# Optimization experiments

Measured on AMD Instinct MI355X. Metric: run time of the kernel, lower is better.

## Reference

```python
import jax, jax.numpy as jnp
import numpy as np


def setup_inputs() -> dict:
    key = jax.random.key(0)
    k1, k2, k3 = jax.random.split(key, 3)
    B, R, C = 8, 4096, 1024
    input_dim = 1024
    weight_params = jax.random.normal(k1, (B, R, C), dtype=jnp.float32)
    logits = jax.random.normal(k2, (B, input_dim), dtype=jnp.float32)
    score_w = jax.random.normal(k3, (input_dim, 1), dtype=jnp.float32) * (1.0 / np.sqrt(input_dim))
    score_b = jnp.zeros((1,), dtype=jnp.float32)
    return {"weight_params": weight_params, "logits": logits, "score_w": score_w, "score_b": score_b}


def reference(weight_params, logits, score_w, score_b):
    # score_generator: Linear(input_dim -> 1), then sigmoid -> keep fraction
    keep_fraction = jax.nn.sigmoid(logits @ score_w + score_b)  # [B, 1]
    total_row_count = weight_params.shape[-2]
    rows_to_keep = jnp.clip(
        (keep_fraction * total_row_count).astype(jnp.int32), 1, None
    ).squeeze(-1)  # [B]
    # per-row L2 magnitudes
    row_magnitudes = jnp.linalg.norm(weight_params, axis=-1)  # [B, R]
    # descending sort, pick the k-th largest magnitude as threshold
    sorted_magnitudes = jnp.sort(row_magnitudes, axis=-1)[..., ::-1]  # [B, R]
    thresholds = jnp.take_along_axis(
        sorted_magnitudes, (rows_to_keep - 1)[:, None], axis=-1
    )  # [B, 1]
    top_k_row_mask = (row_magnitudes >= thresholds).astype(weight_params.dtype)  # [B, R]
    return weight_params * top_k_row_mask[..., None]
```

## Files before the change

### kernel.cpp

```cpp
#include <hip/hip_runtime.h>
#include <hip/hip_bf16.h>
#include <math.h>

#define B 8
#define R 4096
#define C 1024
#define NROWS (B * R)
#define F4_PER_ROW (C / 4)

typedef float vfloat4 __attribute__((ext_vector_type(4)));

__global__ void k_mags(const float* __restrict__ wp,
                       float* __restrict__ mags) {
    int row  = blockIdx.x * 4 + (threadIdx.x >> 6);
    int lane = threadIdx.x & 63;
    const vfloat4* p = (const vfloat4*)(wp + (size_t)row * C);
    double acc = 0.0;
#pragma unroll
    for (int j = 0; j < 4; ++j) {
        vfloat4 v = p[j * 64 + lane];
        acc += (double)v.x * v.x + (double)v.y * v.y +
               (double)v.z * v.z + (double)v.w * v.w;
    }
    for (int off = 32; off > 0; off >>= 1)
        acc += __shfl_down(acc, off, 64);
    if (lane == 0) mags[row] = (float)sqrt(acc);
}

__global__ void k_select(const float* __restrict__ logits,
                         const float* __restrict__ sw,
                         const float* __restrict__ sb,
                         const float* __restrict__ mags,
                         float* __restrict__ thr) {
    __shared__ unsigned hist[256];
    __shared__ double dred[16];
    __shared__ unsigned sh_prefix;
    __shared__ int sh_krem;

    const int b = blockIdx.x, t = threadIdx.x;
    const int wave = t >> 6, lane = t & 63;

    double a = (double)logits[b * C + t] * (double)sw[t];
    for (int off = 32; off > 0; off >>= 1)
        a += __shfl_down(a, off, 64);
    if (lane == 0) dred[wave] = a;
    __syncthreads();
    if (t == 0) {
        double s = (double)sb[0];
        for (int w = 0; w < 16; ++w) s += dred[w];
        double kf = 1.0 / (1.0 + exp(-s));
        int k = (int)(kf * (double)R);
        if (k < 1) k = 1;
        if (k > R) k = R;
        sh_krem = k;
        sh_prefix = 0u;
    }

    unsigned u[4];
#pragma unroll
    for (int j = 0; j < 4; ++j)
        u[j] = __float_as_uint(mags[b * R + t + j * 1024]);
    __syncthreads();

    const int shifts[4] = {24, 16, 8, 0};
    const unsigned maskH[4] = {0x00000000u, 0xFF000000u, 0xFFFF0000u, 0xFFFFFF00u};
#pragma unroll
    for (int p = 0; p < 4; ++p) {
        const int shift = shifts[p];
        const unsigned mh = maskH[p];
        if (t < 256) hist[t] = 0u;
        __syncthreads();
        const unsigned pref = sh_prefix;
        const int krem = sh_krem;
#pragma unroll
        for (int j = 0; j < 4; ++j) {
            if ((u[j] & mh) == pref)
                atomicAdd(&hist[(u[j] >> shift) & 255u], 1u);
        }
        __syncthreads();
        if (t < 64) {
            unsigned h0 = hist[4 * t], h1 = hist[4 * t + 1],
                     h2 = hist[4 * t + 2], h3 = hist[4 * t + 3];
            unsigned s4 = h0 + h1 + h2 + h3;
            unsigned suf = s4;
            for (int off = 1; off < 64; off <<= 1) {
                unsigned tmp = __shfl_down(suf, off, 64);
                if (lane + off < 64) suf += tmp;
            }
            unsigned below = suf - s4;
            if ((int)suf >= krem && (int)below < krem) {
                unsigned hh[4] = {h0, h1, h2, h3};
                unsigned cum = below;
                for (int bb = 3; bb >= 0; --bb) {
                    cum += hh[bb];
                    if ((int)cum >= krem) {
                        sh_krem   = krem - (int)(cum - hh[bb]);
                        sh_prefix = pref | ((unsigned)(4 * t + bb) << shift);
                        break;
                    }
                }
            }
        }
        __syncthreads();
    }
    if (t == 0) thr[b] = __uint_as_float(sh_prefix);
}

__global__ void k_apply(const float* __restrict__ wp,
                        const float* __restrict__ mags,
                        const float* __restrict__ thr,
                        float* __restrict__ out) {
    const int t = threadIdx.x;
    const int row0 = blockIdx.x * 8;
    const int b = row0 >> 12;
    const float tb = thr[b];
    const vfloat4* src = ((const vfloat4*)wp) + (size_t)row0 * F4_PER_ROW;
    vfloat4*       dst = ((vfloat4*)out)      + (size_t)row0 * F4_PER_ROW;
#pragma unroll
    for (int j = 0; j < 8; ++j) {
        if (mags[row0 + j] >= tb) {
            vfloat4 v = src[j * F4_PER_ROW + t];
            __builtin_nontemporal_store(v, &dst[j * F4_PER_ROW + t]);
        } else {
            vfloat4 z = {0.0f, 0.0f, 0.0f, 0.0f};
            __builtin_nontemporal_store(z, &dst[j * F4_PER_ROW + t]);
        }
    }
}

extern "C" void kernel_launch(void* const* d_in, const int* in_sizes, int n_in,
                              void* d_out, int out_size, void* d_ws, size_t ws_size,
                              hipStream_t stream) {
    const float* wp     = (const float*)d_in[0];
    const float* logits = (const float*)d_in[1];
    const float* sw     = (const float*)d_in[2];
    const float* sb     = (const float*)d_in[3];
    float* out = (float*)d_out;

    float* mags = (float*)d_ws;
    float* thr  = mags + NROWS;

    k_mags  <<<NROWS / 4, 256, 0, stream>>>(wp, mags);
    k_select<<<B, 1024, 0, stream>>>(logits, sw, sb, mags, thr);
    k_apply <<<NROWS / 8, 256, 0, stream>>>(wp, mags, thr, out);
}
```

Measured before the change: 244.0 us.

## Fuse radix-select into magnitude kernel via last-block-done atomic counter

Moves the keep-count computation into a small init kernel and merges the per-batch radix select into the magnitude kernel. Each block bumps a per-batch atomic counter, and the last block to finish for a batch runs the 4-pass histogram select with 256 threads over 16 values each. This removes the separate select kernel, which ran only 8 blocks, and its launch gap. The cost is a threadfence plus atomic in every block and a serial tail done by whichever block finishes last.

```diff
diff --git a/kernel.cpp b/kernel.cpp
--- a/kernel.cpp
+++ b/kernel.cpp
@@ -1,5 +1,4 @@
 #include <hip/hip_runtime.h>
-#include <hip/hip_bf16.h>
 #include <math.h>
 
 #define B 8
@@ -7,13 +6,53 @@
 #define C 1024
 #define NROWS (B * R)
 #define F4_PER_ROW (C / 4)
+#define BLOCKS_PER_BATCH 1024
 
 typedef float vfloat4 __attribute__((ext_vector_type(4)));
 
-__global__ void k_mags(const float* __restrict__ wp,
-                       float* __restrict__ mags) {
-    int row  = blockIdx.x * 4 + (threadIdx.x >> 6);
-    int lane = threadIdx.x & 63;
+__global__ void k_init(const float* __restrict__ logits,
+                       const float* __restrict__ sw,
+                       const float* __restrict__ sb,
+                       unsigned* __restrict__ cnt,
+                       int* __restrict__ kkeep) {
+    const int b = blockIdx.x, t = threadIdx.x;
+    if (t == 0) cnt[b] = 0u;
+    double a = 0.0;
+#pragma unroll
+    for (int j = 0; j < 8; ++j) {
+        const int idx = t + j * 128;
+        a += (double)logits[b * C + idx] * (double)sw[idx];
+    }
+    for (int off = 32; off > 0; off >>= 1)
+        a += __shfl_down(a, off, 64);
+    __shared__ double dred[2];
+    if ((t & 63) == 0) dred[t >> 6] = a;
+    __syncthreads();
+    if (t == 0) {
+        double s = (double)sb[0] + dred[0] + dred[1];
+        double kf = 1.0 / (1.0 + exp(-s));
+        int k = (int)(kf * (double)R);
+        if (k < 1) k = 1;
+        if (k > R) k = R;
+        kkeep[b] = k;
+    }
+}
+
+__global__ void k_mags_select(const float* __restrict__ wp,
+                              float* __restrict__ mags,
+                              unsigned* __restrict__ cnt,
+                              const int* __restrict__ kkeep,
+                              float* __restrict__ thr) {
+    __shared__ unsigned s_old;
+    __shared__ unsigned hist[256];
+    __shared__ unsigned sh_prefix;
+    __shared__ int sh_krem;
+
+    const int t    = threadIdx.x;
+    const int row  = blockIdx.x * 4 + (t >> 6);
+    const int lane = t & 63;
+    const int b    = blockIdx.x >> 10;
+
     const vfloat4* p = (const vfloat4*)(wp + (size_t)row * C);
     double acc = 0.0;
 #pragma unroll
@@ -25,55 +64,39 @@
     for (int off = 32; off > 0; off >>= 1)
         acc += __shfl_down(acc, off, 64);
     if (lane == 0) mags[row] = (float)sqrt(acc);
-}
 
-__global__ void k_select(const float* __restrict__ logits,
-                         const float* __restrict__ sw,
-                         const float* __restrict__ sb,
-                         const float* __restrict__ mags,
-                         float* __restrict__ thr) {
-    __shared__ unsigned hist[256];
-    __shared__ double dred[16];
-    __shared__ unsigned sh_prefix;
-    __shared__ int sh_krem;
-
-    const int b = blockIdx.x, t = threadIdx.x;
-    const int wave = t >> 6, lane = t & 63;
-
-    double a = (double)logits[b * C + t] * (double)sw[t];
-    for (int off = 32; off > 0; off >>= 1)
-        a += __shfl_down(a, off, 64);
-    if (lane == 0) dred[wave] = a;
     __syncthreads();
     if (t == 0) {
-        double s = (double)sb[0];
-        for (int w = 0; w < 16; ++w) s += dred[w];
-        double kf = 1.0 / (1.0 + exp(-s));
-        int k = (int)(kf * (double)R);
-        if (k < 1) k = 1;
-        if (k > R) k = R;
-        sh_krem = k;
+        __threadfence();
+        s_old = atomicAdd(&cnt[b], 1u);
+    }
+    __syncthreads();
+    if (s_old != BLOCKS_PER_BATCH - 1u) return;
+
+    __threadfence();
+
+    unsigned u[16];
+#pragma unroll
+    for (int j = 0; j < 16; ++j)
+        u[j] = __float_as_uint(mags[b * R + t + j * 256]);
+
+    if (t == 0) {
         sh_prefix = 0u;
+        sh_krem   = kkeep[b];
     }
-
-    unsigned u[4];
-#pragma unroll
-    for (int j = 0; j < 4; ++j)
-        u[j] = __float_as_uint(mags[b * R + t + j * 1024]);
-    __syncthreads();
 
     const int shifts[4] = {24, 16, 8, 0};
     const unsigned maskH[4] = {0x00000000u, 0xFF000000u, 0xFFFF0000u, 0xFFFFFF00u};
 #pragma unroll
-    for (int p = 0; p < 4; ++p) {
-        const int shift = shifts[p];
-        const unsigned mh = maskH[p];
-        if (t < 256) hist[t] = 0u;
+    for (int p4 = 0; p4 < 4; ++p4) {
+        const int shift = shifts[p4];
+        const unsigned mh = maskH[p4];
+        hist[t] = 0u;
         __syncthreads();
         const unsigned pref = sh_prefix;
         const int krem = sh_krem;
 #pragma unroll
-        for (int j = 0; j < 4; ++j) {
+        for (int j = 0; j < 16; ++j) {
             if ((u[j] & mh) == pref)
                 atomicAdd(&hist[(u[j] >> shift) & 255u], 1u);
         }
@@ -85,7 +108,7 @@
             unsigned suf = s4;
             for (int off = 1; off < 64; off <<= 1) {
                 unsigned tmp = __shfl_down(suf, off, 64);
-                if (lane + off < 64) suf += tmp;
+                if ((t & 63) + off < 64) suf += tmp;
             }
             unsigned below = suf - s4;
             if ((int)suf >= krem && (int)below < krem) {
@@ -137,10 +160,12 @@
     const float* sb     = (const float*)d_in[3];
     float* out = (float*)d_out;
 
-    float* mags = (float*)d_ws;
-    float* thr  = mags + NROWS;
+    float*    mags  = (float*)d_ws;
+    float*    thr   = mags + NROWS;
+    unsigned* cnt   = (unsigned*)(thr + B);
+    int*      kkeep = (int*)(cnt + B);
 
-    k_mags  <<<NROWS / 4, 256, 0, stream>>>(wp, mags);
-    k_select<<<B, 1024, 0, stream>>>(logits, sw, sb, mags, thr);
-    k_apply <<<NROWS / 8, 256, 0, stream>>>(wp, mags, thr, out);
+    k_init       <<<B, 128, 0, stream>>>(logits, sw, sb, cnt, kkeep);
+    k_mags_select<<<NROWS / 4, 256, 0, stream>>>(wp, mags, cnt, kkeep, thr);
+    k_apply      <<<NROWS / 8, 256, 0, stream>>>(wp, mags, thr, out);
 }
```

Measured after the change: 614.2 us. 2.52x slower.
